# Performance work log

Measured on AMD Instinct MI355X. Metric: run time of the kernel, lower is better.

Reference implementation:

```python
import jax, jax.numpy as jnp
import numpy as np

D_MODEL = 256
K_NEIGHBORS = 16
SCALE = 1.0 / np.sqrt(D_MODEL).astype(np.float32)


def setup_inputs() -> dict:
    key = jax.random.key(0)
    k1, k2 = jax.random.split(key)
    B, N = 4, 4096
    xyz = jax.random.normal(k1, (B, N, 3), dtype=jnp.float32)
    features = jax.random.normal(k2, (B, N, D_MODEL), dtype=jnp.float32)
    return {"xyz": xyz, "features": features}


def reference(xyz, features):
    B, N, _ = xyz.shape
    # Squared pairwise distances (same ordering as torch.cdist p=2, so
    # identical top-k indices without the sqrt).
    sq = jnp.sum(xyz * xyz, axis=-1)  # (B, N)
    d2 = sq[:, :, None] + sq[:, None, :] - 2.0 * jnp.einsum('bnc,bmc->bnm', xyz, xyz)
    # k+1 smallest (self included), then drop self (the nearest).
    _, knn_idx = jax.lax.top_k(-d2, K_NEIGHBORS + 1)  # (B, N, k+1)
    knn_idx = knn_idx[..., 1:]                         # (B, N, k)
    # Gather neighbor features: (B, N, k, d)
    knn_feats = jax.vmap(lambda f, idx: f[idx])(features, knn_idx)
    # Per-atom attention over its k neighbors.
    scores = jnp.einsum('bnd,bnkd->bnk', features, knn_feats) * SCALE
    weights = jax.nn.softmax(scores, axis=-1)
    out = jnp.einsum('bnk,bnkd->bnd', weights, knn_feats)
    return out
```

## Files before the change

### kernel.cpp

```cpp
#include <hip/hip_runtime.h>
#include <stdint.h>

#define N_PTS 4096
#define B_SZ 4
#define D_MODEL 256
#define K_NB 16
#define K1 17

__device__ __forceinline__ uint64_t bcast_u64(uint64_t v, int srclane) {
    const int sl = __builtin_amdgcn_readfirstlane(srclane);
    const uint32_t lo = (uint32_t)__builtin_amdgcn_readlane((int)(uint32_t)v, sl);
    const uint32_t hi = (uint32_t)__builtin_amdgcn_readlane((int)(v >> 32), sl);
    return ((uint64_t)hi << 32) | lo;
}

__device__ __forceinline__ uint64_t shfl_up1_u64(uint64_t v) {
    const uint32_t lo = (uint32_t)__shfl_up((int)(uint32_t)v, 1, 64);
    const uint32_t hi = (uint32_t)__shfl_up((int)(v >> 32), 1, 64);
    return ((uint64_t)hi << 32) | lo;
}

__device__ __forceinline__ uint32_t f32_mono(float f) {
    uint32_t u = __float_as_uint(f);
    return (u & 0x80000000u) ? ~u : (u | 0x80000000u);
}

__global__ __launch_bounds__(256) void knn_attn_kernel(
    const float* __restrict__ xyz, const float* __restrict__ feat,
    float* __restrict__ out)
{
    const int lane = threadIdx.x & 63;
    const int q = (int)((blockIdx.x * blockDim.x + threadIdx.x) >> 6);
    const int b = q >> 12;
    const int n = q & (N_PTS - 1);

    const float* xb = xyz + (size_t)b * N_PTS * 3;

    const float xn = xb[3 * n + 0];
    const float yn = xb[3 * n + 1];
    const float zn = xb[3 * n + 2];
    const float sqn = __fadd_rn(__fadd_rn(__fmul_rn(xn, xn), __fmul_rn(yn, yn)),
                                __fmul_rn(zn, zn));

    uint64_t held = ~0ull;
    uint64_t thr  = ~0ull;

    for (int s = 0; s < N_PTS / 64; ++s) {
        const int j = s * 64 + lane;
        const float cx = xb[3 * j + 0];
        const float cy = xb[3 * j + 1];
        const float cz = xb[3 * j + 2];
        const float sqc = __fadd_rn(
            __fadd_rn(__fmul_rn(cx, cx), __fmul_rn(cy, cy)), __fmul_rn(cz, cz));
        const float dt = __fadd_rn(
            __fadd_rn(__fmul_rn(cx, xn), __fmul_rn(cy, yn)), __fmul_rn(cz, zn));
        const float d2 = __fsub_rn(__fadd_rn(sqn, sqc), __fmul_rn(2.0f, dt));
        const uint64_t key = ((uint64_t)f32_mono(d2) << 32) | (uint32_t)j;

        uint64_t pass = __ballot(key < thr);
        while (pass) {
            const int L = (int)__ffsll((unsigned long long)pass) - 1;
            pass &= pass - 1;
            const uint64_t K = bcast_u64(key, L);
            if (K < thr) {
                uint64_t prev = shfl_up1_u64(held);
                prev = (lane == 0) ? 0ull : prev;
                held = (held <= K) ? held : ((prev <= K) ? K : prev);
                thr = bcast_u64(held, 16);
            }
        }
    }

    const int myidx = (int)(uint32_t)held;

    const float* fb = feat + (size_t)b * N_PTS * D_MODEL;
    const float4 qf = *(const float4*)(fb + (size_t)n * D_MODEL + lane * 4);

    float4 vf[K_NB];
    float sc[K_NB];
#pragma unroll
    for (int k = 0; k < K_NB; ++k) {
        const int nbr = __shfl(myidx, k + 1, 64);
        vf[k] = *(const float4*)(fb + (size_t)nbr * D_MODEL + lane * 4);
        float p = qf.x * vf[k].x + qf.y * vf[k].y + qf.z * vf[k].z + qf.w * vf[k].w;
#pragma unroll
        for (int o = 1; o < 64; o <<= 1) p += __shfl_xor(p, o, 64);
        sc[k] = p * 0.0625f;
    }

    float mx = sc[0];
#pragma unroll
    for (int k = 1; k < K_NB; ++k) mx = fmaxf(mx, sc[k]);
    float se = 0.0f;
#pragma unroll
    for (int k = 0; k < K_NB; ++k) {
        sc[k] = __expf(sc[k] - mx);
        se += sc[k];
    }
    const float inv = 1.0f / se;

    float4 acc = make_float4(0.f, 0.f, 0.f, 0.f);
#pragma unroll
    for (int k = 0; k < K_NB; ++k) {
        const float w = sc[k] * inv;
        acc.x += w * vf[k].x;
        acc.y += w * vf[k].y;
        acc.z += w * vf[k].z;
        acc.w += w * vf[k].w;
    }
    *(float4*)(out + (size_t)q * D_MODEL + lane * 4) = acc;
}

extern "C" void kernel_launch(void* const* d_in, const int* in_sizes, int n_in,
                              void* d_out, int out_size, void* d_ws, size_t ws_size,
                              hipStream_t stream) {
    const float* xyz  = (const float*)d_in[0];
    const float* feat = (const float*)d_in[1];
    float* out = (float*)d_out;

    const int n_queries = B_SZ * N_PTS;
    const int threads = 256;
    const int blocks = n_queries * 64 / threads;
    knn_attn_kernel<<<blocks, threads, 0, stream>>>(xyz, feat, out);
}
```

Measured before the change: 204.6 us.

## Seed kNN list with bitonic sort and use float threshold filtering

The first 64 candidates are now sorted with a wave-level bitonic network to seed the held list, replacing 64 serial insertions. The per-chunk filter compares the float distance against a float threshold read once per chunk. Inside the loop, insertions no longer re-check or re-broadcast the threshold after each insert. Because the threshold is stale within a chunk and the test uses <=, some extra insertions may run, which should be harmless for correctness given the ordered insert, while cutting the broadcast and readlane overhead.

```diff
diff --git a/kernel.cpp b/kernel.cpp
--- a/kernel.cpp
+++ b/kernel.cpp
@@ -5,12 +5,10 @@
 #define B_SZ 4
 #define D_MODEL 256
 #define K_NB 16
-#define K1 17
 
-__device__ __forceinline__ uint64_t bcast_u64(uint64_t v, int srclane) {
-    const int sl = __builtin_amdgcn_readfirstlane(srclane);
-    const uint32_t lo = (uint32_t)__builtin_amdgcn_readlane((int)(uint32_t)v, sl);
-    const uint32_t hi = (uint32_t)__builtin_amdgcn_readlane((int)(v >> 32), sl);
+__device__ __forceinline__ uint64_t shfl_xor_u64(uint64_t v, int m) {
+    const uint32_t lo = (uint32_t)__shfl_xor((int)(uint32_t)v, m, 64);
+    const uint32_t hi = (uint32_t)__shfl_xor((int)(v >> 32), m, 64);
     return ((uint64_t)hi << 32) | lo;
 }
 
@@ -20,9 +18,12 @@
     return ((uint64_t)hi << 32) | lo;
 }
 
-__device__ __forceinline__ uint32_t f32_mono(float f) {
-    uint32_t u = __float_as_uint(f);
+__device__ __forceinline__ uint32_t f32_mono(uint32_t u) {
     return (u & 0x80000000u) ? ~u : (u | 0x80000000u);
+}
+__device__ __forceinline__ float mono_to_f32(uint32_t m) {
+    const uint32_t u = (m & 0x80000000u) ? (m ^ 0x80000000u) : ~m;
+    return __uint_as_float(u);
 }
 
 __global__ __launch_bounds__(256) void knn_attn_kernel(
@@ -42,10 +43,36 @@
     const float sqn = __fadd_rn(__fadd_rn(__fmul_rn(xn, xn), __fmul_rn(yn, yn)),
                                 __fmul_rn(zn, zn));
 
-    uint64_t held = ~0ull;
-    uint64_t thr  = ~0ull;
+    uint64_t held;
 
-    for (int s = 0; s < N_PTS / 64; ++s) {
+    {
+        const float cx = xb[3 * lane + 0];
+        const float cy = xb[3 * lane + 1];
+        const float cz = xb[3 * lane + 2];
+        const float sqc = __fadd_rn(
+            __fadd_rn(__fmul_rn(cx, cx), __fmul_rn(cy, cy)), __fmul_rn(cz, cz));
+        const float dt = __fadd_rn(
+            __fadd_rn(__fmul_rn(cx, xn), __fmul_rn(cy, yn)), __fmul_rn(cz, zn));
+        const float d2 = __fsub_rn(__fadd_rn(sqn, sqc), __fmul_rn(2.0f, dt));
+        uint64_t key = ((uint64_t)f32_mono(__float_as_uint(d2)) << 32)
+                       | (uint32_t)lane;
+#pragma unroll
+        for (int k = 2; k <= 64; k <<= 1) {
+#pragma unroll
+            for (int j2 = k >> 1; j2 > 0; j2 >>= 1) {
+                const uint64_t o = shfl_xor_u64(key, j2);
+                const bool keepMin =
+                    (((lane & j2) == 0) == ((lane & k) == 0));
+                const bool c = o < key;
+                key = (c == keepMin) ? o : key;
+            }
+        }
+        held = key;
+    }
+    float thr_f = mono_to_f32(
+        (uint32_t)__builtin_amdgcn_readlane((int)(held >> 32), 16));
+
+    for (int s = 1; s < N_PTS / 64; ++s) {
         const int j = s * 64 + lane;
         const float cx = xb[3 * j + 0];
         const float cy = xb[3 * j + 1];
@@ -55,19 +82,23 @@
         const float dt = __fadd_rn(
             __fadd_rn(__fmul_rn(cx, xn), __fmul_rn(cy, yn)), __fmul_rn(cz, zn));
         const float d2 = __fsub_rn(__fadd_rn(sqn, sqc), __fmul_rn(2.0f, dt));
-        const uint64_t key = ((uint64_t)f32_mono(d2) << 32) | (uint32_t)j;
 
-        uint64_t pass = __ballot(key < thr);
-        while (pass) {
-            const int L = (int)__ffsll((unsigned long long)pass) - 1;
-            pass &= pass - 1;
-            const uint64_t K = bcast_u64(key, L);
-            if (K < thr) {
+        uint64_t pass = __ballot(d2 <= thr_f);
+        if (pass) {
+            const uint32_t d2u = __float_as_uint(d2);
+            do {
+                const int L = (int)__ffsll((unsigned long long)pass) - 1;
+                pass &= pass - 1;
+                const uint32_t ru =
+                    (uint32_t)__builtin_amdgcn_readlane((int)d2u, L);
+                const uint64_t K = ((uint64_t)f32_mono(ru) << 32)
+                                   | (uint32_t)(s * 64 + L);
                 uint64_t prev = shfl_up1_u64(held);
                 prev = (lane == 0) ? 0ull : prev;
                 held = (held <= K) ? held : ((prev <= K) ? K : prev);
-                thr = bcast_u64(held, 16);
-            }
+            } while (pass);
+            thr_f = mono_to_f32(
+                (uint32_t)__builtin_amdgcn_readlane((int)(held >> 32), 16));
         }
     }
 
```

Result: faster. 176.3 us (-13.8%).
